# Kernel optimization log

Hardware: AMD Instinct MI355X
Metric: run time of the kernel (lower is better)

Reference implementation:

```python
import jax, jax.numpy as jnp
import numpy as np

B, T, NHANDS, DKP = 8, 1024, 2, 128
DM, H, DH, DFF, V, M, L = 1024, 16, 64, 4096, 2000, 256, 2
KEPS = 1e-4  # performer feature-map epsilon


def _orth_proj(key, m, d):
    # Gaussian orthogonal random features (FAVOR+), rows rescaled to chi norms
    n_blocks = int(np.ceil(m / d))
    blocks = []
    for i in range(n_blocks):
        q, _ = jnp.linalg.qr(jax.random.normal(jax.random.fold_in(key, i), (d, d)))
        blocks.append(q.T)
    mat = jnp.concatenate(blocks, 0)[:m]
    mult = jnp.linalg.norm(jax.random.normal(jax.random.fold_in(key, 10 ** 6), (m, d)), axis=1)
    return (mat * mult[:, None]).astype(jnp.float32)


def setup_inputs() -> dict:
    key = jax.random.key(0)
    ks = iter(jax.random.split(key, 64))
    w = lambda shape, s=0.02: (jax.random.normal(next(ks), shape) * s).astype(jnp.float32)
    z = lambda *shape: jnp.zeros(shape, jnp.float32)
    o = lambda *shape: jnp.ones(shape, jnp.float32)
    return {
        'x': jax.random.normal(next(ks), (B, T, NHANDS, DKP), dtype=jnp.float32),
        'Win': w((NHANDS * DKP, DM)), 'b_in': z(DM),
        'pe': jax.random.normal(next(ks), (5000, DM), dtype=jnp.float32),
        'ln1_g': o(L, DM), 'ln1_b': z(L, DM),
        'Wq': w((L, DM, DM)), 'bq': z(L, DM),
        'Wk': w((L, DM, DM)), 'bk': z(L, DM),
        'Wv': w((L, DM, DM)), 'bv': z(L, DM),
        'Wo': w((L, DM, DM)), 'bo': z(L, DM),
        'ln2_g': o(L, DM), 'ln2_b': z(L, DM),
        'W1': w((L, DM, DFF)), 'b1': z(L, DFF),
        'W2': w((L, DFF, DM)), 'b2': z(L, DM),
        'Wc': w((DM, V)), 'bc': z(V),
        'Wconv': w((64, DM, 3)), 'bconv': z(64),
        'Waux': w((64, V + 1)), 'baux': z(V + 1),
        'proj': _orth_proj(next(ks), M, DH),
    }


def _ln(x, g, b):
    mu = jnp.mean(x, -1, keepdims=True)
    var = jnp.mean((x - mu) ** 2, -1, keepdims=True)
    return (x - mu) / jnp.sqrt(var + 1e-5) * g + b


def _feats(data, proj, is_query):
    # FAVOR+ softmax kernel features, data: (B,H,T,DH) -> (B,H,T,M)
    dn = DH ** -0.25
    ratio = M ** -0.5
    dd = jnp.einsum('bhnd,md->bhnm', data, proj) * dn
    diag = jnp.sum(data ** 2, -1, keepdims=True) * 0.5 * dn * dn
    if is_query:
        stab = jnp.max(dd, -1, keepdims=True)
    else:
        stab = jnp.max(dd, (-1, -2), keepdims=True)
    return ratio * (jnp.exp(dd - diag - jax.lax.stop_gradient(stab)) + KEPS)


def reference(x, Win, b_in, pe, ln1_g, ln1_b, Wq, bq, Wk, bk, Wv, bv, Wo, bo,
              ln2_g, ln2_b, W1, b1, W2, b2, Wc, bc, Wconv, bconv, Waux, baux, proj):
    h = x.reshape(B, T, NHANDS * DKP) @ Win + b_in
    h = h + pe[:T][None]

    def layer(h, i):
        y = _ln(h, ln1_g[i], ln1_b[i])
        q = (y @ Wq[i] + bq[i]).reshape(B, T, H, DH).transpose(0, 2, 1, 3)
        k = (y @ Wk[i] + bk[i]).reshape(B, T, H, DH).transpose(0, 2, 1, 3)
        v = (y @ Wv[i] + bv[i]).reshape(B, T, H, DH).transpose(0, 2, 1, 3)
        qp = _feats(q, proj, True)   # (B,H,T,M)
        kp = _feats(k, proj, False)
        dinv = 1.0 / jnp.einsum('bhnm,bhm->bhn', qp, kp.sum(2))
        ctx = jnp.einsum('bhnm,bhnd->bhmd', kp, v)          # (B,H,M,DH)
        o = jnp.einsum('bhnm,bhmd->bhnd', qp, ctx) * dinv[..., None]
        o = o.transpose(0, 2, 1, 3).reshape(B, T, DM) @ Wo[i] + bo[i]
        h = h + o
        y = _ln(h, ln2_g[i], ln2_b[i])
        ff = jax.nn.gelu(y @ W1[i] + b1[i], approximate=False) @ W2[i] + b2[i]
        return h + ff

    h = layer(h, 0)
    xa = h.transpose(0, 2, 1)  # (B, DM, T)
    xa = jax.lax.conv_general_dilated(xa, Wconv, (1,), 'SAME',
                                      dimension_numbers=('NCH', 'OIH', 'NCH'))
    xa = xa + bconv[None, :, None]
    aux = xa.transpose(0, 2, 1) @ Waux + baux  # (B, T, V+1)
    h = layer(h, 1)
    gloss = h @ Wc + bc  # (B, T, V)
    return (gloss, aux)
```

## Files before the change

### kernel.cpp

```cpp
#include <hip/hip_runtime.h>
#include <hip/hip_bf16.h>

typedef __attribute__((ext_vector_type(4))) float f32x4;
typedef __attribute__((ext_vector_type(8))) unsigned short u16x8;
typedef __attribute__((ext_vector_type(4))) unsigned short u16x4;
typedef __bf16 bf16x8 __attribute__((ext_vector_type(8)));

#define DEVFN static __device__ __forceinline__

constexpr int CB = 8, CT = 1024, CDM = 1024, CH = 16, CDH = 64, CDFF = 4096, CV = 2000, CM = 256;
constexpr int CNT = CB * CT;
constexpr int CQKV = 3072;
constexpr float CDN = 0.35355339059327373f;
constexpr float CRATIO = 0.0625f;
constexpr float CKEPS = 1e-4f;

DEVFN unsigned short f2bu(float x) {
  __hip_bfloat16 h = __float2bfloat16(x);
  return __builtin_bit_cast(unsigned short, h);
}
DEVFN float b2f(unsigned short u) {
  __hip_bfloat16 h = __builtin_bit_cast(__hip_bfloat16, u);
  return __bfloat162float(h);
}
DEVFN float wredsum(float s) {
#pragma unroll
  for (int ofs = 32; ofs; ofs >>= 1) s += __shfl_xor(s, ofs, 64);
  return s;
}
DEVFN float wredmax(float s) {
#pragma unroll
  for (int ofs = 32; ofs; ofs >>= 1) s = fmaxf(s, __shfl_xor(s, ofs, 64));
  return s;
}
DEVFN void gl_lds16(const void* g, void* l) {
  __builtin_amdgcn_global_load_lds(
      (const __attribute__((address_space(1))) unsigned int*)g,
      (__attribute__((address_space(3))) unsigned int*)l, 16, 0, 0);
}
DEVFN f32x4 mfma16(u16x8 a, u16x8 b, f32x4 c) {
  return __builtin_amdgcn_mfma_f32_16x16x32_bf16(
      __builtin_bit_cast(bf16x8, a), __builtin_bit_cast(bf16x8, b), c, 0, 0, 0);
}
DEVFN u16x8 lds_rd128(unsigned addr) {
  u16x8 r;
  asm volatile("ds_read_b128 %0, %1" : "=v"(r) : "v"(addr));
  return r;
}
DEVFN unsigned lds_addr(const void* p) {
  return (unsigned)(unsigned long)(const __attribute__((address_space(3))) char*)p;
}

#define EPI_BIAS 1
#define EPI_ACCUM 2
#define EPI_GELU 4
#define EPI_OUTBF 8
#define EPI_RSCALE 16

template <int EPI>
__global__ __launch_bounds__(512, 4) void gemm128_k(
    const unsigned short* __restrict__ A, const unsigned short* __restrict__ Bt,
    const float* __restrict__ bias, void* __restrict__ C,
    int Mr, int Nr, int Kr, int lda, int ldb, int ldc) {
  __shared__ unsigned short smA[2][128 * 64];
  __shared__ unsigned short smB[2][128 * 64];

  int tid = threadIdx.x, wv = tid >> 6, ll = tid & 63;
  int wm = wv >> 2, wn = wv & 3;
  int m0 = blockIdx.x * 128, n0 = blockIdx.y * 128;
  int fr = ll & 15, f16 = ll >> 4, fk = f16 * 8;

  const char* Ab = (const char*)A;
  const char* Bb = (const char*)Bt;

  unsigned int offA[2], offB[2];
#pragma unroll
  for (int ro = 0; ro < 2; ro++) {
    int L = (ro * 512 + tid) * 16;
    int P = L ^ (((L >> 9) & 1) << 5);
    int kh = P >> 13, rem = P & 8191;
    int r = rem >> 6, cb = rem & 63;
    long rowA = min(m0 + r, Mr - 1);
    offA[ro] = (unsigned)((rowA * lda + kh * 32) * 2 + cb);
    long rowB = min(n0 + r, Nr - 1);
    offB[ro] = (unsigned)((rowB * ldb + kh * 32) * 2 + cb);
  }
  unsigned aAb = lds_addr(&smA[0][0]), aBb = lds_addr(&smB[0][0]);
  unsigned offArd[4], offBrd[2];
#pragma unroll
  for (int i = 0; i < 4; i++) {
    int r = wm * 64 + i * 16 + fr;
    offArd[i] = aAb + (unsigned)(r * 64 + 2 * (fk ^ (((r >> 3) & 1) << 4)));
  }
#pragma unroll
  for (int j = 0; j < 2; j++) {
    int r = wn * 32 + j * 16 + fr;
    offBrd[j] = aBb + (unsigned)(r * 64 + 2 * (fk ^ (((r >> 3) & 1) << 4)));
  }

  f32x4 acc[4][2] = {};
  int NT = Kr / 64;

#define STGALL(PB, KBN)                                                      \
  {                                                                          \
    _Pragma("unroll") for (int ro = 0; ro < 2; ro++)                         \
        gl_lds16(Ab + offA[ro] + (KBN), &smA[PB][(ro * 512 + wv * 64) * 8]); \
    _Pragma("unroll") for (int ro = 0; ro < 2; ro++)                         \
        gl_lds16(Bb + offB[ro] + (KBN), &smB[PB][(ro * 512 + wv * 64) * 8]); \
  }
#define TILE(PB, KBN)                                                        \
  {                                                                          \
    __builtin_amdgcn_s_barrier();              \
    __builtin_amdgcn_sched_barrier(0);                                       \
    STGALL((PB) ^ 1, KBN);                                                   \
    asm volatile("s_waitcnt vmcnt(4)" ::: "memory");                         \
    __builtin_amdgcn_sched_barrier(0);                                       \
    __builtin_amdgcn_s_barrier();                 \
    __builtin_amdgcn_sched_barrier(0);                                       \
    u16x8 a0[4], b0[2], a1[4], b1[2];                                        \
    _Pragma("unroll") for (int i = 0; i < 4; i++)                            \
        a0[i] = lds_rd128(offArd[i] + (PB)*16384);                           \
    _Pragma("unroll") for (int j = 0; j < 2; j++)                            \
        b0[j] = lds_rd128(offBrd[j] + (PB)*16384);                           \
    _Pragma("unroll") for (int i = 0; i < 4; i++)                            \
        a1[i] = lds_rd128(offArd[i] + (PB)*16384 + 8192);                    \
    _Pragma("unroll") for (int j = 0; j < 2; j++)                            \
        b1[j] = lds_rd128(offBrd[j] + (PB)*16384 + 8192);                    \
    asm volatile("s_waitcnt lgkmcnt(6)" ::: "memory");                       \
    __builtin_amdgcn_sched_barrier(0);                                       \
    __builtin_amdgcn_s_setprio(1);                                           \
    _Pragma("unroll") for (int i = 0; i < 4; i++) {                          \
      acc[i][0] = mfma16(a0[i], b0[0], acc[i][0]);                           \
      acc[i][1] = mfma16(a0[i], b0[1], acc[i][1]);                           \
    }                                                                        \
    __builtin_amdgcn_s_setprio(0);                                           \
    asm volatile("s_waitcnt lgkmcnt(0)" ::: "memory");                       \
    __builtin_amdgcn_sched_barrier(0);                                       \
    __builtin_amdgcn_s_setprio(1);                                           \
    _Pragma("unroll") for (int i = 0; i < 4; i++) {                          \
      acc[i][0] = mfma16(a1[i], b1[0], acc[i][0]);                           \
      acc[i][1] = mfma16(a1[i], b1[1], acc[i][1]);                           \
    }                                                                        \
    __builtin_amdgcn_s_setprio(0);                                           \
  }

  STGALL(0, 0);
  for (int t = 0; t < NT; t += 2) {
    long kb1 = (long)(t + 1) * 128;
    long kb2 = (long)min(t + 2, NT - 1) * 128;
    TILE(0, kb1);
    TILE(1, kb2);
  }
  asm volatile("s_waitcnt vmcnt(0)" ::: "memory");
  __builtin_amdgcn_sched_barrier(0);
#undef TILE
#undef STGALL

#pragma unroll
  for (int i = 0; i < 4; i++) {
#pragma unroll
    for (int j = 0; j < 2; j++) {
#pragma unroll
      for (int e = 0; e < 4; e++) {
        int gr = m0 + wm * 64 + i * 16 + f16 * 4 + e;
        int gc = n0 + wn * 32 + j * 16 + fr;
        if (gr < Mr && gc < Nr) {
          float v = acc[i][j][e];
          if (EPI & EPI_BIAS) v += bias[gc];
          if (EPI & EPI_GELU) v = 0.5f * v * (1.0f + erff(v * 0.70710678118f));
          long idx = (long)gr * ldc + gc;
          if (EPI & EPI_ACCUM) v += ((float*)C)[idx];
          if (EPI & EPI_OUTBF) ((unsigned short*)C)[idx] = f2bu(v);
          else ((float*)C)[idx] = v;
        }
      }
    }
  }
}

template <int EPI, int MB, int NB>
__global__ __launch_bounds__(256) void gemm_k(
    const unsigned short* __restrict__ Aall, const unsigned short* __restrict__ Btall,
    const float* __restrict__ bias, void* __restrict__ Call, const float* __restrict__ rsall,
    int Mr, int Nr, int Kr, int lda, int ldb, int ldc, int bdiv,
    long As1, long As2, long Bs1, long Bs2, long Cs1, long Cs2, long Rs1, long Rs2) {
  __shared__ unsigned short smA[MB * 32];
  __shared__ unsigned short smB[NB * 32];
  constexpr int WRN = (MB == 128 && NB == 128) ? 2 : (MB == 128 ? 4 : 1);
  constexpr int WCN = 4 / WRN;
  constexpr int MT = MB / WRN, NTW = NB / WCN;
  constexpr int AF = MT / 16, BF = NTW / 16;
  int bz = blockIdx.z;
  const unsigned short* A = Aall + (long)(bz / bdiv) * As1 + (long)(bz % bdiv) * As2;
  const unsigned short* Bt = Btall + (long)(bz / bdiv) * Bs1 + (long)(bz % bdiv) * Bs2;
  long coff = (long)(bz / bdiv) * Cs1 + (long)(bz % bdiv) * Cs2;
  const float* rs = nullptr;
  if (EPI & EPI_RSCALE) rs = rsall + (long)(bz / bdiv) * Rs1 + (long)(bz % bdiv) * Rs2;

  int tid = threadIdx.x, wv = tid >> 6, ll = tid & 63;
  int m0 = blockIdx.x * MB, n0 = blockIdx.y * NB;
  int sr = tid >> 2, sc = (tid & 3) * 8;
  long ar0 = min(m0 + sr, Mr - 1);
  long ar1 = (MB == 128) ? min(m0 + sr + 64, (long)Mr - 1) : 0;
  long br0 = min(n0 + sr, Nr - 1);
  long br1 = (NB == 128) ? min(n0 + sr + 64, (long)Nr - 1) : 0;
  unsigned short* lA0 = &smA[(wv * 16) * 32];
  unsigned short* lA1 = &smA[(64 + wv * 16) * 32];
  unsigned short* lB0 = &smB[(wv * 16) * 32];
  unsigned short* lB1 = &smB[(64 + wv * 16) * 32];

  f32x4 acc[AF][BF] = {};
  int wr = (WRN == 1) ? 0 : ((WRN == 2) ? (wv >> 1) * MT : wv * MT);
  int wc = (WCN == 1) ? 0 : ((WCN == 2) ? (wv & 1) * NTW : wv * NTW);
  int fr = ll & 15, fk = (ll >> 4) * 8;

  for (int k0 = 0; k0 < Kr; k0 += 32) {
    __syncthreads();
    gl_lds16(A + ar0 * lda + k0 + sc, lA0);
    if (MB == 128) gl_lds16(A + ar1 * lda + k0 + sc, lA1);
    gl_lds16(Bt + br0 * ldb + k0 + sc, lB0);
    if (NB == 128) gl_lds16(Bt + br1 * ldb + k0 + sc, lB1);
    __syncthreads();
    u16x8 af[AF], bfr[BF];
#pragma unroll
    for (int i = 0; i < AF; i++) af[i] = *(const u16x8*)&smA[(wr + i * 16 + fr) * 32 + fk];
#pragma unroll
    for (int j = 0; j < BF; j++) bfr[j] = *(const u16x8*)&smB[(wc + j * 16 + fr) * 32 + fk];
#pragma unroll
    for (int i = 0; i < AF; i++)
#pragma unroll
      for (int j = 0; j < BF; j++) acc[i][j] = mfma16(af[i], bfr[j], acc[i][j]);
  }

#pragma unroll
  for (int i = 0; i < AF; i++) {
#pragma unroll
    for (int j = 0; j < BF; j++) {
#pragma unroll
      for (int e = 0; e < 4; e++) {
        int gr = m0 + wr + i * 16 + (ll >> 4) * 4 + e;
        int gc = n0 + wc + j * 16 + (ll & 15);
        if (gr < Mr && gc < Nr) {
          float v = acc[i][j][e];
          if (EPI & EPI_BIAS) v += bias[gc];
          if (EPI & EPI_GELU) v = 0.5f * v * (1.0f + erff(v * 0.70710678118f));
          if (EPI & EPI_RSCALE) v *= rs[gr];
          long idx = coff + (long)gr * ldc + gc;
          if (EPI & EPI_ACCUM) v += ((float*)Call)[idx];
          if (EPI & EPI_OUTBF) ((unsigned short*)Call)[idx] = f2bu(v);
          else ((float*)Call)[idx] = v;
        }
      }
    }
  }
}

DEVFN void feat_dd(const unsigned short* __restrict__ src, const unsigned short* __restrict__ projc,
                   unsigned short* ldsq, unsigned short* ldsp, int b, int t0, int hh,
                   f32x4 acc[16]) {
  int tid = threadIdx.x, wv = tid >> 6, ll = tid & 63;
#pragma unroll
  for (int p = 0; p < 2; p++) {
    int r = p * 64 + (tid >> 3), c8 = (tid & 7) * 8;
    *(u16x8*)&ldsq[r * 72 + c8] =
        *(const u16x8*)&src[((long)b * CT + t0 + r) * CQKV + hh * CDH + c8];
  }
#pragma unroll
  for (int p = 0; p < 4; p++) {
    int r = p * 64 + (tid >> 3), c8 = (tid & 7) * 8;
    *(u16x8*)&ldsp[r * 72 + c8] = *(const u16x8*)&projc[r * 64 + c8];
  }
  __syncthreads();
  int fr = ll & 15, fk = (ll >> 4) * 8;
#pragma unroll
  for (int ks = 0; ks < 2; ks++) {
    u16x8 af = *(const u16x8*)&ldsq[(wv * 16 + fr) * 72 + ks * 32 + fk];
#pragma unroll
    for (int j = 0; j < 16; j++) {
      u16x8 bf = *(const u16x8*)&ldsp[(j * 16 + fr) * 72 + ks * 32 + fk];
      acc[j] = mfma16(af, bf, acc[j]);
    }
  }
}

__global__ __launch_bounds__(512, 4) void kstab_f(const unsigned short* __restrict__ kb,
                                                  const unsigned short* __restrict__ projc,
                                                  float* __restrict__ part) {
  extern __shared__ char dynsm[];
  unsigned short* ldsq = (unsigned short*)dynsm;
  unsigned short* ldsp = (unsigned short*)(dynsm + 18432);
  __shared__ float smx[8];
  int bh = blockIdx.x >> 3, chunk = blockIdx.x & 7;
  int b = bh >> 4, hh = bh & 15;
  f32x4 acc[16] = {};
  feat_dd(kb, projc, ldsq, ldsp, b, chunk * 128, hh, acc);
  float mx = -3.4e38f;
#pragma unroll
  for (int j = 0; j < 16; j++)
#pragma unroll
    for (int e = 0; e < 4; e++) mx = fmaxf(mx, acc[j][e]);
  mx = wredmax(mx);
  int wv = threadIdx.x >> 6;
  if ((threadIdx.x & 63) == 0) smx[wv] = mx;
  __syncthreads();
  if (threadIdx.x == 0) {
    float m2 = smx[0];
#pragma unroll
    for (int i = 1; i < 8; i++) m2 = fmaxf(m2, smx[i]);
    part[blockIdx.x] = m2;
  }
}

__global__ __launch_bounds__(512, 4) void featk_f(const unsigned short* __restrict__ kb,
                                                  const unsigned short* __restrict__ projc,
                                                  const float* __restrict__ part,
                                                  unsigned short* __restrict__ kpt,
                                                  float* __restrict__ kspart) {
  extern __shared__ char dynsm[];
  unsigned short* ldsq = (unsigned short*)dynsm;
  unsigned short* ldsp = (unsigned short*)(dynsm + 18432);
  unsigned short* ldso = (unsigned short*)dynsm;
  int tid = threadIdx.x, wv = tid >> 6, ll = tid & 63;
  int bh = blockIdx.x >> 3, chunk = blockIdx.x & 7;
  int b = bh >> 4, hh = bh & 15;
  float st = part[bh * 8];
#pragma unroll
  for (int i = 1; i < 8; i++) st = fmaxf(st, part[bh * 8 + i]);
  f32x4 acc[16] = {};
  feat_dd(kb, projc, ldsq, ldsp, b, chunk * 128, hh, acc);
  int fr = ll & 15, g = ll >> 4;
  float diag[4];
#pragma unroll
  for (int e = 0; e < 4; e++) {
    int row = wv * 16 + g * 4 + e;
    u16x4 kv = *(const u16x4*)&ldsq[row * 72 + fr * 4];
    float s = 0;
#pragma unroll
    for (int z = 0; z < 4; z++) { float f = b2f(kv[z]); s += f * f; }
#pragma unroll
    for (int o = 1; o < 16; o <<= 1) s += __shfl_xor(s, o, 64);
    diag[e] = s * (0.5f * CDN * CDN);
  }
  __syncthreads();
#pragma unroll
  for (int j = 0; j < 16; j++)
#pragma unroll
    for (int e = 0; e < 4; e++) {
      float v = CRATIO * (expf(acc[j][e] - diag[e] - st) + CKEPS);
      ldso[(j * 16 + fr) * 136 + wv * 16 + g * 4 + e] = f2bu(v);
    }
  __syncthreads();
  int m = tid >> 1, seg = (tid & 1) * 64;
  long base = ((long)bh * CM + m) * CT + chunk * 128;
  float ks = 0;
#pragma unroll
  for (int z = 0; z < 8; z++) {
    u16x8 v8 = *(u16x8*)&ldso[m * 136 + seg + z * 8];
    *(u16x8*)&kpt[base + seg + z * 8] = v8;
#pragma unroll
    for (int w = 0; w < 8; w++) ks += b2f(v8[w]);
  }
  ks += __shfl_xor(ks, 1, 64);
  if ((tid & 1) == 0) kspart[((long)bh * 8 + chunk) * CM + m] = ks;
}

__global__ __launch_bounds__(256) void ksred_k(const float* __restrict__ kspart,
                                               float* __restrict__ ksum) {
  int i = blockIdx.x * 256 + threadIdx.x;
  int bh = i >> 8, m = i & 255;
  float s = 0;
#pragma unroll
  for (int c = 0; c < 8; c++) s += kspart[((long)bh * 8 + c) * CM + m];
  ksum[i] = s;
}

__global__ __launch_bounds__(512, 4) void featq_f(const unsigned short* __restrict__ qb,
                                                  const unsigned short* __restrict__ projc,
                                                  const float* __restrict__ ksum,
                                                  unsigned short* __restrict__ qp,
                                                  float* __restrict__ dinv) {
  extern __shared__ char dynsm[];
  unsigned short* ldsq = (unsigned short*)dynsm;
  unsigned short* ldsp = (unsigned short*)(dynsm + 18432);
  unsigned short* ldso = (unsigned short*)dynsm;
  float* ldks = (float*)(dynsm + 67584);
  int tid = threadIdx.x, wv = tid >> 6, ll = tid & 63;
  int bh = blockIdx.x >> 3, chunk = blockIdx.x & 7;
  int b = bh >> 4, hh = bh & 15;
  int t0 = chunk * 128;
  if (tid < 256) ldks[tid] = ksum[bh * CM + tid];
  f32x4 acc[16] = {};
  feat_dd(qb, projc, ldsq, ldsp, b, t0, hh, acc);
  int fr = ll & 15, g = ll >> 4;
  float rmax[4], diag[4];
#pragma unroll
  for (int e = 0; e < 4; e++) {
    float mx = acc[0][e];
#pragma unroll
    for (int j = 1; j < 16; j++) mx = fmaxf(mx, acc[j][e]);
#pragma unroll
    for (int o = 1; o < 16; o <<= 1) mx = fmaxf(mx, __shfl_xor(mx, o, 64));
    rmax[e] = mx;
    int row = wv * 16 + g * 4 + e;
    u16x4 qv = *(const u16x4*)&ldsq[row * 72 + fr * 4];
    float s = 0;
#pragma unroll
    for (int z = 0; z < 4; z++) { float f = b2f(qv[z]); s += f * f; }
#pragma unroll
    for (int o = 1; o < 16; o <<= 1) s += __shfl_xor(s, o, 64);
    diag[e] = s * (0.5f * CDN * CDN);
  }
  __syncthreads();
#pragma unroll
  for (int j = 0; j < 16; j++)
#pragma unroll
    for (int e = 0; e < 4; e++) {
      float v = CRATIO * (expf(acc[j][e] - diag[e] - rmax[e]) + CKEPS);
      ldso[(wv * 16 + g * 4 + e) * 264 + j * 16 + fr] = f2bu(v);
    }
  __syncthreads();
  int row = tid >> 2, seg = (tid & 3) * 64;
  long base = ((long)bh * CT + t0) * CM;
  float dot = 0;
#pragma unroll
  for (int z = 0; z < 8; z++) {
    u16x8 v8 = *(u16x8*)&ldso[row * 264 + seg + z * 8];
    *(u16x8*)&qp[base + (long)row * CM + seg + z * 8] = v8;
#pragma unroll
    for (int w = 0; w < 8; w++) dot += b2f(v8[w]) * ldks[seg + z * 8 + w];
  }
  dot += __shfl_xor(dot, 1, 64);
  dot += __shfl_xor(dot, 2, 64);
  if ((tid & 3) == 0) dinv[(long)bh * CT + t0 + row] = 1.0f / dot;
}

__global__ __launch_bounds__(256) void ln_k(const float* __restrict__ h,
                                            const float* __restrict__ g,
                                            const float* __restrict__ b,
                                            unsigned short* __restrict__ y) {
  int wv = threadIdx.x >> 6, ll = threadIdx.x & 63;
  long row = (long)blockIdx.x * 4 + wv;
  const float* hr = h + row * CDM;
  f32x4 x[4];
#pragma unroll
  for (int i = 0; i < 4; i++) x[i] = *(const f32x4*)&hr[ll * 16 + i * 4];
  float s = 0;
#pragma unroll
  for (int i = 0; i < 4; i++)
#pragma unroll
    for (int e = 0; e < 4; e++) s += x[i][e];
  float mu = wredsum(s) * (1.f / CDM);
  float v = 0;
#pragma unroll
  for (int i = 0; i < 4; i++)
#pragma unroll
    for (int e = 0; e < 4; e++) {
      float d = x[i][e] - mu;
      v += d * d;
    }
  float inv = rsqrtf(wredsum(v) * (1.f / CDM) + 1e-5f);
  unsigned short o[16];
#pragma unroll
  for (int i = 0; i < 4; i++)
#pragma unroll
    for (int e = 0; e < 4; e++) {
      int c = ll * 16 + i * 4 + e;
      o[i * 4 + e] = f2bu((x[i][e] - mu) * inv * g[c] + b[c]);
    }
  *(u16x8*)&y[row * CDM + ll * 16] = *(u16x8*)&o[0];
  *(u16x8*)&y[row * CDM + ll * 16 + 8] = *(u16x8*)&o[8];
}

__global__ __launch_bounds__(256) void trv_k(const unsigned short* __restrict__ vb,
                                             unsigned short* __restrict__ vt) {
  int bh = blockIdx.x >> 5;
  int t0 = (blockIdx.x & 31) * 32;
  int b = bh >> 4, hh = bh & 15;
  __shared__ unsigned short tile[32][64];
  int tr = threadIdx.x >> 3, dblk = (threadIdx.x & 7) * 8;
  *(u16x8*)&tile[tr][dblk] = *(const u16x8*)&vb[((long)b * CT + t0 + tr) * CQKV + hh * CDH + dblk];
  __syncthreads();
  int d = threadIdx.x >> 2, tz = (threadIdx.x & 3) * 8;
  unsigned short o[8];
#pragma unroll
  for (int e = 0; e < 8; e++) o[e] = tile[tz + e][d];
  *(u16x8*)&vt[((long)bh * CDH + d) * CT + t0 + tz] = *(u16x8*)&o[0];
}

__global__ __launch_bounds__(256) void addpe_k(float* __restrict__ h, const float* __restrict__ pe) {
  long i = ((long)blockIdx.x * 256 + threadIdx.x) * 4;
  int t = (int)((i >> 10) & 1023);
  int c = (int)(i & 1023);
  f32x4 v = *(f32x4*)&h[i];
  f32x4 p = *(const f32x4*)&pe[(long)t * 1024 + c];
  v += p;
  *(f32x4*)&h[i] = v;
}

__global__ __launch_bounds__(256) void f2b_k(const float* __restrict__ in,
                                             unsigned short* __restrict__ out, long n) {
  long i = ((long)blockIdx.x * 256 + threadIdx.x) * 4;
  if (i >= n) return;
  f32x4 v = *(const f32x4*)&in[i];
  unsigned short o[4];
#pragma unroll
  for (int e = 0; e < 4; e++) o[e] = f2bu(v[e]);
  *(u16x4*)&out[i] = *(u16x4*)&o[0];
}

__global__ __launch_bounds__(256) void tconv_k(const float* __restrict__ in,
                                               unsigned short* __restrict__ out, int R, int C) {
  __shared__ float tile[32][33];
  int r0 = blockIdx.x * 32, c0 = blockIdx.y * 32;
  int tr = threadIdx.x >> 5, tc = threadIdx.x & 31;
#pragma unroll
  for (int p = 0; p < 4; p++) {
    int r = r0 + p * 8 + tr, c = c0 + tc;
    tile[p * 8 + tr][tc] = (r < R && c < C) ? in[(long)r * C + c] : 0.f;
  }
  __syncthreads();
#pragma unroll
  for (int p = 0; p < 4; p++) {
    int c = c0 + p * 8 + tr, r = r0 + tc;
    if (c < C && r < R) out[(long)c * R + r] = f2bu(tile[tc][p * 8 + tr]);
  }
}

__global__ __launch_bounds__(256) void wconv_k(const float* __restrict__ W,
                                               unsigned short* __restrict__ out) {
  int idx = blockIdx.x * 256 + threadIdx.x;
  int r = idx >> 16, rem = idx & 65535, oc = rem >> 10, ic = rem & 1023;
  out[idx] = f2bu(W[oc * 3072 + ic * 3 + r]);
}

__global__ __launch_bounds__(256) void convmix_k(const float* __restrict__ Y,
                                                 const float* __restrict__ bc,
                                                 float* __restrict__ xa) {
  long t = (long)blockIdx.x * 4 + (threadIdx.x >> 6);
  int oc = threadIdx.x & 63;
  long tm = t > 0 ? t - 1 : 0, tp = t < CNT - 1 ? t + 1 : CNT - 1;
  float v = Y[tm * 192 + oc] + Y[t * 192 + 64 + oc] + Y[tp * 192 + 128 + oc] + bc[oc];
  xa[t * 64 + oc] = v;
}

__global__ __launch_bounds__(256) void projc_k(const float* __restrict__ p,
                                               unsigned short* __restrict__ out) {
  int i = blockIdx.x * 256 + threadIdx.x;
  out[i] = f2bu(p[i] * CDN);
}

__global__ __launch_bounds__(256) void catb_k(const float* __restrict__ q,
                                              const float* __restrict__ k,
                                              const float* __restrict__ v,
                                              float* __restrict__ o) {
  int i = blockIdx.x * 256 + threadIdx.x;
  o[i] = i < 1024 ? q[i] : (i < 2048 ? k[i - 1024] : v[i - 2048]);
}

__global__ __launch_bounds__(256) void patch_k(const float* __restrict__ h,
                                               const float* __restrict__ W,
                                               const float* __restrict__ bc,
                                               float* __restrict__ xa) {
  int b = blockIdx.x >> 1;
  int t = (blockIdx.x & 1) ? (CT - 1) : 0;
  int oc = threadIdx.x & 63, ch = threadIdx.x >> 6;
  float s = 0;
  for (int r = 0; r < 3; r++) {
    int tt = t + r - 1;
    if (tt < 0 || tt >= CT) continue;
    const float* hr = h + ((long)b * CT + tt) * CDM;
    const float* wr = W + oc * 3072 + r;
    for (int ic = ch * 256; ic < ch * 256 + 256; ic++) s += hr[ic] * wr[ic * 3];
  }
  __shared__ float sm[256];
  sm[threadIdx.x] = s;
  __syncthreads();
  if (threadIdx.x < 64) {
    float tot = sm[oc] + sm[64 + oc] + sm[128 + oc] + sm[192 + oc] + bc[oc];
    xa[((long)b * CT + t) * 64 + oc] = tot;
  }
}

#define LAUNCH_GEMM(EPI, MB, NB, A, Bt, bias, C, rsp, Mr, Nr, Kr, lda, ldb, ldc, nb, bdiv, As1, As2, Bs1, Bs2, Cs1, Cs2, Rs1, Rs2) \
  gemm_k<EPI, MB, NB><<<dim3(((Mr) + (MB)-1) / (MB), ((Nr) + (NB)-1) / (NB), (nb)), 256, 0, stream>>>( \
      (const unsigned short*)(A), (const unsigned short*)(Bt), (bias), (void*)(C), (rsp),        \
      (Mr), (Nr), (Kr), (lda), (ldb), (ldc), (bdiv), (long)(As1), (long)(As2), (long)(Bs1),      \
      (long)(Bs2), (long)(Cs1), (long)(Cs2), (long)(Rs1), (long)(Rs2))

#define LAUNCH_G1(EPI, A, Bt, bias, C, Mr, Nr, Kr, lda, ldb, ldc)                                \
  gemm128_k<EPI><<<dim3(((Mr) + 127) / 128, ((Nr) + 127) / 128), 512, 0, stream>>>(              \
      (const unsigned short*)(A), (const unsigned short*)(Bt), (bias), (void*)(C),               \
      (Mr), (Nr), (Kr), (lda), (ldb), (ldc))

extern "C" void kernel_launch(void* const* d_in, const int* in_sizes, int n_in,
                              void* d_out, int out_size, void* d_ws, size_t ws_size,
                              hipStream_t stream) {
  const float* x = (const float*)d_in[0];
  const float* Win = (const float*)d_in[1];
  const float* b_in = (const float*)d_in[2];
  const float* pe = (const float*)d_in[3];
  const float* ln1_g = (const float*)d_in[4];
  const float* ln1_b = (const float*)d_in[5];
  const float* Wq = (const float*)d_in[6];
  const float* bq = (const float*)d_in[7];
  const float* Wk = (const float*)d_in[8];
  const float* bk = (const float*)d_in[9];
  const float* Wv = (const float*)d_in[10];
  const float* bv = (const float*)d_in[11];
  const float* Wo = (const float*)d_in[12];
  const float* bo = (const float*)d_in[13];
  const float* ln2_g = (const float*)d_in[14];
  const float* ln2_b = (const float*)d_in[15];
  const float* W1 = (const float*)d_in[16];
  const float* b1 = (const float*)d_in[17];
  const float* W2 = (const float*)d_in[18];
  const float* b2 = (const float*)d_in[19];
  const float* Wc = (const float*)d_in[20];
  const float* bc = (const float*)d_in[21];
  const float* Wconv = (const float*)d_in[22];
  const float* bconv = (const float*)d_in[23];
  const float* Waux = (const float*)d_in[24];
  const float* baux = (const float*)d_in[25];
  const float* proj = (const float*)d_in[26];
  float* out = (float*)d_out;

  char* wsp = (char*)d_ws;
  size_t off = 0;
  auto take = [&](size_t bytes) {
    char* p = wsp + off;
    off = (off + bytes + 255) & ~(size_t)255;
    return p;
  };
  float* h_f = (float*)take(33554432);
  unsigned short* y_bf = (unsigned short*)take(16777216);
  unsigned short* qkv_bf = (unsigned short*)take(50331648);
  unsigned short* qp_bf = (unsigned short*)take(67108864);
  unsigned short* kpt_bf = (unsigned short*)take(67108864);
  unsigned short* ff_bf = (unsigned short*)take(67108864);
  unsigned short* ctx_bf = (unsigned short*)take(4194304);
  float* ksum_f = (float*)take(131072);
  float* kspart_f = (float*)take(1048576);
  float* kstab_f_buf = (float*)take(4096);
  float* dinv_f = (float*)take(524288);
  float* xa_f = (float*)take(2097152);
  float* ycv_f = (float*)take(6291456);
  unsigned short* xabf = (unsigned short*)take(1048576);
  float* bqkv_f = (float*)take(24576);
  unsigned short* hbf = (unsigned short*)take(16777216);
  unsigned short* xbf = (unsigned short*)take(4194304);
  unsigned short* win_t = (unsigned short*)take(524288);
  unsigned short* wqkvo_t = (unsigned short*)take(16777216);
  unsigned short* w1_t = (unsigned short*)take(16777216);
  unsigned short* w2_t = (unsigned short*)take(16777216);
  unsigned short* wc_t = (unsigned short*)take(4096000);
  unsigned short* projc = (unsigned short*)take(32768);
  unsigned short* wconv_t = (unsigned short*)take(393216);
  unsigned short* waux_t = (unsigned short*)take(256128);
  unsigned short* vt_bf = y_bf;
  unsigned short* o_bf = y_bf;
  (void)in_sizes; (void)n_in; (void)out_size; (void)ws_size;

  f2b_k<<<2048, 256, 0, stream>>>(x, xbf, (long)CNT * 256);
  tconv_k<<<dim3(8, 32), 256, 0, stream>>>(Win, win_t, 256, 1024);
  for (int l = 0; l < 2; l++) {
    tconv_k<<<dim3(32, 32), 256, 0, stream>>>(Wq + (long)l * 1048576, wqkvo_t + (long)(l * 4 + 0) * 1048576, 1024, 1024);
    tconv_k<<<dim3(32, 32), 256, 0, stream>>>(Wk + (long)l * 1048576, wqkvo_t + (long)(l * 4 + 1) * 1048576, 1024, 1024);
    tconv_k<<<dim3(32, 32), 256, 0, stream>>>(Wv + (long)l * 1048576, wqkvo_t + (long)(l * 4 + 2) * 1048576, 1024, 1024);
    tconv_k<<<dim3(32, 32), 256, 0, stream>>>(Wo + (long)l * 1048576, wqkvo_t + (long)(l * 4 + 3) * 1048576, 1024, 1024);
    tconv_k<<<dim3(32, 128), 256, 0, stream>>>(W1 + (long)l * 4194304, w1_t + (long)l * 4194304, 1024, 4096);
    tconv_k<<<dim3(128, 32), 256, 0, stream>>>(W2 + (long)l * 4194304, w2_t + (long)l * 4194304, 4096, 1024);
    catb_k<<<12, 256, 0, stream>>>(bq + l * CDM, bk + l * CDM, bv + l * CDM, bqkv_f + l * CQKV);
  }
  tconv_k<<<dim3(32, 63), 256, 0, stream>>>(Wc, wc_t, 1024, 2000);
  tconv_k<<<dim3(2, 63), 256, 0, stream>>>(Waux, waux_t, 64, 2001);
  wconv_k<<<768, 256, 0, stream>>>(Wconv, wconv_t);
  projc_k<<<64, 256, 0, stream>>>(proj, projc);

  LAUNCH_G1(EPI_BIAS, xbf, win_t, b_in, h_f, CNT, CDM, 256, 256, 256, CDM);
  addpe_k<<<8192, 256, 0, stream>>>(h_f, pe);

  for (int l = 0; l < 2; l++) {
    const unsigned short* wqkv_t = wqkvo_t + (long)(l * 4) * 1048576;
    const unsigned short* wo_t = wqkvo_t + (long)(l * 4 + 3) * 1048576;

    ln_k<<<2048, 256, 0, stream>>>(h_f, ln1_g + l * CDM, ln1_b + l * CDM, y_bf);
    LAUNCH_G1(EPI_BIAS | EPI_OUTBF, y_bf, wqkv_t, bqkv_f + l * CQKV, qkv_bf, CNT, CQKV, CDM, CDM, CDM, CQKV);

    kstab_f<<<1024, 512, 55296, stream>>>(qkv_bf + 1024, projc, kstab_f_buf);
    featk_f<<<1024, 512, 69632, stream>>>(qkv_bf + 1024, projc, kstab_f_buf, kpt_bf, kspart_f);
    ksred_k<<<128, 256, 0, stream>>>(kspart_f, ksum_f);
    featq_f<<<1024, 512, 68608, stream>>>(qkv_bf, projc, ksum_f, qp_bf, dinv_f);
    trv_k<<<4096, 256, 0, stream>>>(qkv_bf + 2048, vt_bf);
    LAUNCH_GEMM(EPI_OUTBF, 64, 128, vt_bf, kpt_bf, nullptr, ctx_bf, nullptr, CDH, CM, CT, CT, CT, CM, 128, CH,
                (long)CH * CDH * CT, (long)CDH * CT, (long)CH * CM * CT, (long)CM * CT,
                (long)CH * CDH * CM, (long)CDH * CM, 0, 0);
    LAUNCH_GEMM(EPI_RSCALE | EPI_OUTBF, 128, 64, qp_bf, ctx_bf, nullptr, o_bf, dinv_f, CT, CDH, CM, CM, CM, CDM, 128, CH,
                (long)CH * CT * CM, (long)CT * CM, (long)CH * CDH * CM, (long)CDH * CM,
                (long)CT * CDM, 64, (long)CH * CT, (long)CT);
    LAUNCH_G1(EPI_BIAS | EPI_ACCUM, o_bf, wo_t, bo + l * CDM, h_f, CNT, CDM, CDM, CDM, CDM, CDM);

    ln_k<<<2048, 256, 0, stream>>>(h_f, ln2_g + l * CDM, ln2_b + l * CDM, y_bf);
    LAUNCH_G1(EPI_BIAS | EPI_GELU | EPI_OUTBF, y_bf, w1_t + (long)l * 4194304, b1 + l * CDFF, ff_bf,
              CNT, CDFF, CDM, CDM, CDM, CDFF);
    LAUNCH_G1(EPI_BIAS | EPI_ACCUM, ff_bf, w2_t + (long)l * 4194304, b2 + l * CDM, h_f,
              CNT, CDM, CDFF, CDFF, CDFF, CDM);

    if (l == 0) {
      f2b_k<<<8192, 256, 0, stream>>>(h_f, hbf, (long)CNT * CDM);
      LAUNCH_GEMM(0, 128, 128, hbf, wconv_t, nullptr, ycv_f, nullptr, CNT, 192, CDM, CDM, CDM, 192, 1, 1, 0, 0, 0, 0, 0, 0, 0, 0);
      convmix_k<<<2048, 256, 0, stream>>>(ycv_f, bconv, xa_f);
      patch_k<<<16, 256, 0, stream>>>(h_f, Wconv, bconv, xa_f);
      f2b_k<<<512, 256, 0, stream>>>(xa_f, xabf, (long)CNT * 64);
      LAUNCH_GEMM(EPI_BIAS, 128, 128, xabf, waux_t, baux, out + 16384000, nullptr, CNT, CV + 1, 64, 64, 64, CV + 1, 1, 1, 0, 0, 0, 0, 0, 0, 0, 0);
    }
  }

  f2b_k<<<8192, 256, 0, stream>>>(h_f, hbf, (long)CNT * CDM);
  LAUNCH_G1(EPI_BIAS, hbf, wc_t, bc, out, CNT, CV, CDM, CDM, CDM, CV);
}
```

Before: 1.310 ms.

## Add 4-wave 64x64-per-wave GEMM for wide QKV and FFN1, batch weight transposes

```diff
diff --git a/kernel.cpp b/kernel.cpp
--- a/kernel.cpp
+++ b/kernel.cpp
@@ -54,8 +54,131 @@
 #define EPI_BIAS 1
 #define EPI_ACCUM 2
 #define EPI_GELU 4
+#define EPI_RSCALE 16
 #define EPI_OUTBF 8
-#define EPI_RSCALE 16
+
+template <int EPI>
+__global__ __launch_bounds__(256, 2) void gemmsq_k(
+    const unsigned short* __restrict__ A, const unsigned short* __restrict__ Bt,
+    const float* __restrict__ bias, void* __restrict__ C,
+    int Mr, int Nr, int Kr, int lda, int ldb, int ldc) {
+  __shared__ unsigned short smA[2][128 * 64];
+  __shared__ unsigned short smB[2][128 * 64];
+
+  int tid = threadIdx.x, wv = tid >> 6, ll = tid & 63;
+  int wm = wv >> 1, wn = wv & 1;
+  int m0 = blockIdx.x * 128, n0 = blockIdx.y * 128;
+  int fr = ll & 15, f16 = ll >> 4, fk = f16 * 8;
+
+  const char* Ab = (const char*)A;
+  const char* Bb = (const char*)Bt;
+
+  unsigned int offA[4], offB[4];
+#pragma unroll
+  for (int ro = 0; ro < 4; ro++) {
+    int L = (ro * 256 + tid) * 16;
+    int P = L ^ (((L >> 9) & 1) << 5);
+    int kh = P >> 13, rem = P & 8191;
+    int r = rem >> 6, cb = rem & 63;
+    long rowA = min(m0 + r, Mr - 1);
+    offA[ro] = (unsigned)((rowA * lda + kh * 32) * 2 + cb);
+    long rowB = min(n0 + r, Nr - 1);
+    offB[ro] = (unsigned)((rowB * ldb + kh * 32) * 2 + cb);
+  }
+  unsigned aAb = lds_addr(&smA[0][0]), aBb = lds_addr(&smB[0][0]);
+  unsigned offArd[4], offBrd[4];
+#pragma unroll
+  for (int i = 0; i < 4; i++) {
+    int r = wm * 64 + i * 16 + fr;
+    offArd[i] = aAb + (unsigned)(r * 64 + 2 * (fk ^ (((r >> 3) & 1) << 4)));
+  }
+#pragma unroll
+  for (int j = 0; j < 4; j++) {
+    int r = wn * 64 + j * 16 + fr;
+    offBrd[j] = aBb + (unsigned)(r * 64 + 2 * (fk ^ (((r >> 3) & 1) << 4)));
+  }
+
+  f32x4 acc[4][4] = {};
+  int NT = Kr / 64;
+
+#define STGALL(PB, KBN)                                                      \
+  {                                                                          \
+    _Pragma("unroll") for (int ro = 0; ro < 4; ro++)                         \
+        gl_lds16(Ab + offA[ro] + (KBN), &smA[PB][(ro * 256 + wv * 64) * 8]); \
+    _Pragma("unroll") for (int ro = 0; ro < 4; ro++)                         \
+        gl_lds16(Bb + offB[ro] + (KBN), &smB[PB][(ro * 256 + wv * 64) * 8]); \
+  }
+#define KSBODY(PB, KS)                                                       \
+  {                                                                          \
+    u16x8 a[4], b[4];                                                        \
+    _Pragma("unroll") for (int i = 0; i < 4; i++)                            \
+        a[i] = lds_rd128(offArd[i] + (PB)*16384 + (KS)*8192);                \
+    _Pragma("unroll") for (int j = 0; j < 4; j++)                            \
+        b[j] = lds_rd128(offBrd[j] + (PB)*16384 + (KS)*8192);                \
+    asm volatile("s_waitcnt lgkmcnt(2)" ::: "memory");                       \
+    __builtin_amdgcn_sched_barrier(0);                                       \
+    __builtin_amdgcn_s_setprio(1);                                           \
+    _Pragma("unroll") for (int i = 0; i < 4; i++) {                          \
+      acc[i][0] = mfma16(a[i], b[0], acc[i][0]);                             \
+      acc[i][1] = mfma16(a[i], b[1], acc[i][1]);                             \
+    }                                                                        \
+    __builtin_amdgcn_s_setprio(0);                                           \
+    asm volatile("s_waitcnt lgkmcnt(0)" ::: "memory");                       \
+    __builtin_amdgcn_sched_barrier(0);                                       \
+    __builtin_amdgcn_s_setprio(1);                                           \
+    _Pragma("unroll") for (int i = 0; i < 4; i++) {                          \
+      acc[i][2] = mfma16(a[i], b[2], acc[i][2]);                             \
+      acc[i][3] = mfma16(a[i], b[3], acc[i][3]);                             \
+    }                                                                        \
+    __builtin_amdgcn_s_setprio(0);                                           \
+  }
+#define TILE(PB, KBN)                                                        \
+  {                                                                          \
+    __builtin_amdgcn_s_barrier();                                            \
+    __builtin_amdgcn_sched_barrier(0);                                       \
+    STGALL((PB) ^ 1, KBN);                                                   \
+    asm volatile("s_waitcnt vmcnt(8)" ::: "memory");                         \
+    __builtin_amdgcn_sched_barrier(0);                                       \
+    __builtin_amdgcn_s_barrier();                                            \
+    __builtin_amdgcn_sched_barrier(0);                                       \
+    KSBODY(PB, 0);                                                           \
+    KSBODY(PB, 1);                                                           \
+  }
+
+  STGALL(0, 0);
+  for (int t = 0; t < NT; t += 2) {
+    long kb1 = (long)(t + 1) * 128;
+    long kb2 = (long)min(t + 2, NT - 1) * 128;
+    TILE(0, kb1);
+    TILE(1, kb2);
+  }
+  asm volatile("s_waitcnt vmcnt(0)" ::: "memory");
+  __builtin_amdgcn_sched_barrier(0);
+#undef TILE
+#undef KSBODY
+#undef STGALL
+
+#pragma unroll
+  for (int i = 0; i < 4; i++) {
+#pragma unroll
+    for (int j = 0; j < 4; j++) {
+#pragma unroll
+      for (int e = 0; e < 4; e++) {
+        int gr = m0 + wm * 64 + i * 16 + f16 * 4 + e;
+        int gc = n0 + wn * 64 + j * 16 + fr;
+        if (gr < Mr && gc < Nr) {
+          float v = acc[i][j][e];
+          if (EPI & EPI_BIAS) v += bias[gc];
+          if (EPI & EPI_GELU) v = 0.5f * v * (1.0f + erff(v * 0.70710678118f));
+          long idx = (long)gr * ldc + gc;
+          if (EPI & EPI_ACCUM) v += ((float*)C)[idx];
+          if (EPI & EPI_OUTBF) ((unsigned short*)C)[idx] = f2bu(v);
+          else ((float*)C)[idx] = v;
+        }
+      }
+    }
+  }
+}
 
 template <int EPI>
 __global__ __launch_bounds__(512, 4) void gemm128_k(
@@ -110,12 +233,12 @@
   }
 #define TILE(PB, KBN)                                                        \
   {                                                                          \
-    __builtin_amdgcn_s_barrier();              \
+    __builtin_amdgcn_s_barrier();                                            \
     __builtin_amdgcn_sched_barrier(0);                                       \
     STGALL((PB) ^ 1, KBN);                                                   \
     asm volatile("s_waitcnt vmcnt(4)" ::: "memory");                         \
     __builtin_amdgcn_sched_barrier(0);                                       \
-    __builtin_amdgcn_s_barrier();                 \
+    __builtin_amdgcn_s_barrier();                                            \
     __builtin_amdgcn_sched_barrier(0);                                       \
     u16x8 a0[4], b0[2], a1[4], b1[2];                                        \
     _Pragma("unroll") for (int i = 0; i < 4; i++)                            \
@@ -508,21 +631,24 @@
   *(u16x4*)&out[i] = *(u16x4*)&o[0];
 }
 
-__global__ __launch_bounds__(256) void tconv_k(const float* __restrict__ in,
-                                               unsigned short* __restrict__ out, int R, int C) {
+__global__ __launch_bounds__(256) void tconvz_k(const float* __restrict__ in,
+                                                unsigned short* __restrict__ out, int R, int C,
+                                                long szs, long dzs) {
+  const float* src = in + (long)blockIdx.z * szs;
+  unsigned short* dst = out + (long)blockIdx.z * dzs;
   __shared__ float tile[32][33];
   int r0 = blockIdx.x * 32, c0 = blockIdx.y * 32;
   int tr = threadIdx.x >> 5, tc = threadIdx.x & 31;
 #pragma unroll
   for (int p = 0; p < 4; p++) {
     int r = r0 + p * 8 + tr, c = c0 + tc;
-    tile[p * 8 + tr][tc] = (r < R && c < C) ? in[(long)r * C + c] : 0.f;
+    tile[p * 8 + tr][tc] = (r < R && c < C) ? src[(long)r * C + c] : 0.f;
   }
   __syncthreads();
 #pragma unroll
   for (int p = 0; p < 4; p++) {
     int c = c0 + p * 8 + tr, r = r0 + tc;
-    if (c < C && r < R) out[(long)c * R + r] = f2bu(tile[tc][p * 8 + tr]);
+    if (c < C && r < R) dst[(long)c * R + r] = f2bu(tile[tc][p * 8 + tr]);
   }
 }
 
@@ -553,8 +679,10 @@
                                               const float* __restrict__ k,
                                               const float* __restrict__ v,
                                               float* __restrict__ o) {
+  int l = blockIdx.y;
   int i = blockIdx.x * 256 + threadIdx.x;
-  o[i] = i < 1024 ? q[i] : (i < 2048 ? k[i - 1024] : v[i - 2048]);
+  float val = i < 1024 ? q[l * CDM + i] : (i < 2048 ? k[l * CDM + i - 1024] : v[l * CDM + i - 2048]);
+  o[l * CQKV + i] = val;
 }
 
 __global__ __launch_bounds__(256) void patch_k(const float* __restrict__ h,
@@ -589,6 +717,11 @@
 
 #define LAUNCH_G1(EPI, A, Bt, bias, C, Mr, Nr, Kr, lda, ldb, ldc)                                \
   gemm128_k<EPI><<<dim3(((Mr) + 127) / 128, ((Nr) + 127) / 128), 512, 0, stream>>>(              \
+      (const unsigned short*)(A), (const unsigned short*)(Bt), (bias), (void*)(C),               \
+      (Mr), (Nr), (Kr), (lda), (ldb), (ldc))
+
+#define LAUNCH_GS(EPI, A, Bt, bias, C, Mr, Nr, Kr, lda, ldb, ldc)                                \
+  gemmsq_k<EPI><<<dim3(((Mr) + 127) / 128, ((Nr) + 127) / 128), 256, 0, stream>>>(               \
       (const unsigned short*)(A), (const unsigned short*)(Bt), (bias), (void*)(C),               \
       (Mr), (Nr), (Kr), (lda), (ldb), (ldc))
 
@@ -661,18 +794,16 @@
   (void)in_sizes; (void)n_in; (void)out_size; (void)ws_size;
 
   f2b_k<<<2048, 256, 0, stream>>>(x, xbf, (long)CNT * 256);
-  tconv_k<<<dim3(8, 32), 256, 0, stream>>>(Win, win_t, 256, 1024);
-  for (int l = 0; l < 2; l++) {
-    tconv_k<<<dim3(32, 32), 256, 0, stream>>>(Wq + (long)l * 1048576, wqkvo_t + (long)(l * 4 + 0) * 1048576, 1024, 1024);
-    tconv_k<<<dim3(32, 32), 256, 0, stream>>>(Wk + (long)l * 1048576, wqkvo_t + (long)(l * 4 + 1) * 1048576, 1024, 1024);
-    tconv_k<<<dim3(32, 32), 256, 0, stream>>>(Wv + (long)l * 1048576, wqkvo_t + (long)(l * 4 + 2) * 1048576, 1024, 1024);
-    tconv_k<<<dim3(32, 32), 256, 0, stream>>>(Wo + (long)l * 1048576, wqkvo_t + (long)(l * 4 + 3) * 1048576, 1024, 1024);
-    tconv_k<<<dim3(32, 128), 256, 0, stream>>>(W1 + (long)l * 4194304, w1_t + (long)l * 4194304, 1024, 4096);
-    tconv_k<<<dim3(128, 32), 256, 0, stream>>>(W2 + (long)l * 4194304, w2_t + (long)l * 4194304, 4096, 1024);
-    catb_k<<<12, 256, 0, stream>>>(bq + l * CDM, bk + l * CDM, bv + l * CDM, bqkv_f + l * CQKV);
-  }
-  tconv_k<<<dim3(32, 63), 256, 0, stream>>>(Wc, wc_t, 1024, 2000);
-  tconv_k<<<dim3(2, 63), 256, 0, stream>>>(Waux, waux_t, 64, 2001);
+  tconvz_k<<<dim3(8, 32, 1), 256, 0, stream>>>(Win, win_t, 256, 1024, 0, 0);
+  tconvz_k<<<dim3(32, 32, 2), 256, 0, stream>>>(Wq, wqkvo_t + 0 * 1048576, 1024, 1024, 1048576, 4194304);
+  tconvz_k<<<dim3(32, 32, 2), 256, 0, stream>>>(Wk, wqkvo_t + 1 * 1048576, 1024, 1024, 1048576, 4194304);
+  tconvz_k<<<dim3(32, 32, 2), 256, 0, stream>>>(Wv, wqkvo_t + 2 * 1048576, 1024, 1024, 1048576, 4194304);
+  tconvz_k<<<dim3(32, 32, 2), 256, 0, stream>>>(Wo, wqkvo_t + 3 * 1048576, 1024, 1024, 1048576, 4194304);
+  tconvz_k<<<dim3(32, 128, 2), 256, 0, stream>>>(W1, w1_t, 1024, 4096, 4194304, 4194304);
+  tconvz_k<<<dim3(128, 32, 2), 256, 0, stream>>>(W2, w2_t, 4096, 1024, 4194304, 4194304);
+  tconvz_k<<<dim3(32, 63, 1), 256, 0, stream>>>(Wc, wc_t, 1024, 2000, 0, 0);
+  tconvz_k<<<dim3(2, 63, 1), 256, 0, stream>>>(Waux, waux_t, 64, 2001, 0, 0);
+  catb_k<<<dim3(12, 2), 256, 0, stream>>>(bq, bk, bv, bqkv_f);
   wconv_k<<<768, 256, 0, stream>>>(Wconv, wconv_t);
   projc_k<<<64, 256, 0, stream>>>(proj, projc);
 
@@ -684,7 +815,7 @@
     const unsigned short* wo_t = wqkvo_t + (long)(l * 4 + 3) * 1048576;
 
     ln_k<<<2048, 256, 0, stream>>>(h_f, ln1_g + l * CDM, ln1_b + l * CDM, y_bf);
-    LAUNCH_G1(EPI_BIAS | EPI_OUTBF, y_bf, wqkv_t, bqkv_f + l * CQKV, qkv_bf, CNT, CQKV, CDM, CDM, CDM, CQKV);
+    LAUNCH_GS(EPI_BIAS | EPI_OUTBF, y_bf, wqkv_t, bqkv_f + l * CQKV, qkv_bf, CNT, CQKV, CDM, CDM, CDM, CQKV);
 
     kstab_f<<<1024, 512, 55296, stream>>>(qkv_bf + 1024, projc, kstab_f_buf);
     featk_f<<<1024, 512, 69632, stream>>>(qkv_bf + 1024, projc, kstab_f_buf, kpt_bf, kspart_f);
@@ -700,7 +831,7 @@
     LAUNCH_G1(EPI_BIAS | EPI_ACCUM, o_bf, wo_t, bo + l * CDM, h_f, CNT, CDM, CDM, CDM, CDM, CDM);
 
     ln_k<<<2048, 256, 0, stream>>>(h_f, ln2_g + l * CDM, ln2_b + l * CDM, y_bf);
-    LAUNCH_G1(EPI_BIAS | EPI_GELU | EPI_OUTBF, y_bf, w1_t + (long)l * 4194304, b1 + l * CDFF, ff_bf,
+    LAUNCH_GS(EPI_BIAS | EPI_GELU | EPI_OUTBF, y_bf, w1_t + (long)l * 4194304, b1 + l * CDFF, ff_bf,
               CNT, CDFF, CDM, CDM, CDM, CDFF);
     LAUNCH_G1(EPI_BIAS | EPI_ACCUM, ff_bf, w2_t + (long)l * 4194304, b2 + l * CDM, h_f,
               CNT, CDM, CDFF, CDFF, CDFF, CDM);
```

Result: slower. 1.379 ms (+5.3%).
